# Kernel tuning notes

Measured on AMD Instinct MI355X. Metric: run time of the kernel, lower is better.

The kernel has to match this reference:

```python
import jax, jax.numpy as jnp
import numpy as np

EPS = 1e-5          # denominator epsilon from module
PROJ_EPS = 4e-3     # geoopt float32 projection epsilon
MIN_NORM = 1e-15


def _sabs(x):
    return jnp.abs(x) + MIN_NORM


def _sign(x):
    # geoopt sign: sign(0) == 1
    return jnp.sign(jnp.sign(x) + 0.5)


def _clamp_abs(x, eps):
    return _sign(x) * jnp.maximum(jnp.abs(x), eps)


def _lambda_x(x, k):
    # conformal factor 2 / (1 + k ||x||^2)
    return 2.0 / jnp.maximum(1.0 + k * jnp.sum(x * x, axis=-1, keepdims=True), MIN_NORM)


def _parallel_transport0back(x, v, k):
    # transport v at x back to the origin: v / (1 + k ||x||^2)
    return v / jnp.maximum(1.0 + k * jnp.sum(x * x, axis=-1, keepdims=True), MIN_NORM)


def _artan_k(x, k):
    sk = jnp.sqrt(_sabs(k))
    hyp = jnp.arctanh(jnp.minimum(sk * x, 1.0 - 1e-7)) / sk   # k < 0
    sph = jnp.arctan(sk * x) / sk                              # k > 0
    return jnp.where(k < 0, hyp, sph)


def _tan_k(x, k):
    sk = jnp.sqrt(_sabs(k))
    return jnp.where(k < 0, jnp.tanh(sk * x) / sk, jnp.tan(sk * x) / sk)


def _project(x, k):
    maxnorm = (1.0 - PROJ_EPS) / jnp.sqrt(_sabs(k))
    maxnorm = jnp.where(k < 0, maxnorm, 1e15)
    norm = jnp.maximum(jnp.linalg.norm(x, axis=-1, keepdims=True), MIN_NORM)
    return jnp.where(norm > maxnorm, x / norm * maxnorm, x)


def _mobius_scalar_mul(r, x, k):
    xn = jnp.maximum(jnp.linalg.norm(x, axis=-1, keepdims=True), MIN_NORM)
    return _tan_k(r * _artan_k(xn, k), k) * (x / xn)


def setup_inputs() -> dict:
    key = jax.random.key(0)
    kQ, kK, kV = jax.random.split(key, 3)
    B, H, N, D = 4, 16, 4096, 64
    Q = jax.random.normal(kQ, (B, H, N, D), dtype=jnp.float32)
    K = jax.random.normal(kK, (B, H, N, D), dtype=jnp.float32)
    # V holds points on the Poincare ball: scale so ||V|| < 1
    V = 0.05 * jax.random.normal(kV, (B, H, N, D), dtype=jnp.float32)
    mask = jnp.ones((N,), dtype=jnp.float32)
    c = jnp.array([-1.0], dtype=jnp.float32)  # hyperbolic curvature (geoopt k-convention)
    return {"Q": Q, "K": K, "V": V, "mask": mask, "c": c}


def reference(Q, K, V, mask, c):
    H = Q.shape[-3]
    curv = jnp.broadcast_to(c.reshape(-1), (H,)) if c.shape[0] == 1 else c
    curv = curv[:, None, None]  # [H,1,1] broadcasts over [B,H,N,D]

    x = V
    v1 = _parallel_transport0back(x, Q, curv)
    v2 = _parallel_transport0back(x, K, curv)
    gamma = _lambda_x(x, curv)                     # [B,H,N,1]
    denom = _clamp_abs(gamma - 1.0, 1e-10)
    m = mask[None, :, None]                        # [1,N,1]
    x = gamma / denom * x * m
    v1 = jax.nn.elu(v1) + 1.0
    v2 = denom * (jax.nn.elu(v2) + 1.0) * m

    v2_sum = jnp.sum(v2, axis=-2)                  # [B,H,D]
    D = jnp.einsum('...nd,...d->...n', v1, v2_sum)
    D_inv = 1.0 / jnp.where(D == 0, EPS, D)
    context = jnp.einsum('...nd,...ne->...de', v2, x)   # [B,H,D,D]
    X = jnp.einsum('...de,...nd,...n->...ne', context, v1, D_inv)

    X = _project(X, curv)
    X = _mobius_scalar_mul(0.5, X, curv)
    X = _project(X, curv)
    return X
```

## Files before the change

kernel.cpp:

```cpp
#include <hip/hip_runtime.h>
#include <math.h>

#define EPS_C      1e-05f
#define PROJ_EPS_C 0.004f
#define MIN_NORM_C 1e-15f

#define NTOK   4096
#define DH     64
#define TILE   64
#define CHUNK  512
#define NCHUNK (NTOK / CHUNK)
#define PADROW 68

__device__ __forceinline__ float elup(float z) {
    return z > 0.f ? z + 1.f : __expf(z);
}

__global__ __launch_bounds__(256) void glin_phase1(
    const float* __restrict__ Kk, const float* __restrict__ Vv,
    const float* __restrict__ mask, const float* __restrict__ cc,
    int csize, int H,
    float* __restrict__ pt_out, float* __restrict__ v2sum_out,
    float* __restrict__ ctx_out)
{
    __shared__ __align__(16) float v2s[TILE][PADROW];
    __shared__ __align__(16) float xss[TILE][PADROW];

    const int bh    = blockIdx.x;
    const int chunk = blockIdx.y;
    const int h     = bh % H;
    const float k   = cc[(csize == 1) ? 0 : h];

    const float* Kp = Kk + (size_t)bh * NTOK * DH;
    const float* Vp = Vv + (size_t)bh * NTOK * DH;
    float* ptp      = pt_out + (size_t)bh * NTOK;

    const int tid = threadIdx.x;
    const int ty  = tid >> 4;
    const int tx  = tid & 15;

    float acc[4][4];
#pragma unroll
    for (int i = 0; i < 4; ++i)
#pragma unroll
        for (int j = 0; j < 4; ++j) acc[i][j] = 0.f;
    float v2acc[4] = {0.f, 0.f, 0.f, 0.f};

    const int tbase = chunk * CHUNK;
    for (int tt = 0; tt < CHUNK; tt += TILE) {
#pragma unroll
        for (int p = 0; p < 4; ++p) {
            int f   = tid + p * 256;
            int row = f >> 4;
            int c4  = f & 15;
            int gtok = tbase + tt + row;
            float4 v4 = *(const float4*)(Vp + (size_t)gtok * DH + c4 * 4);
            float4 k4 = *(const float4*)(Kp + (size_t)gtok * DH + c4 * 4);
            float ss = v4.x * v4.x + v4.y * v4.y + v4.z * v4.z + v4.w * v4.w;
            ss += __shfl_xor(ss, 1);
            ss += __shfl_xor(ss, 2);
            ss += __shfl_xor(ss, 4);
            ss += __shfl_xor(ss, 8);
            float dpt   = fmaxf(1.f + k * ss, MIN_NORM_C);
            float pt    = 1.f / dpt;
            float gamma = 2.f * pt;
            float gm1   = gamma - 1.f;
            float sg    = (gm1 < 0.f) ? -1.f : 1.f;
            float denomG = sg * fmaxf(fabsf(gm1), 1e-10f);
            float m     = mask[gtok];
            float xsc   = gamma / denomG * m;
            float a2    = denomG * m;
            if (c4 == 0) ptp[gtok] = pt;
            float4 xs4;
            xs4.x = v4.x * xsc; xs4.y = v4.y * xsc;
            xs4.z = v4.z * xsc; xs4.w = v4.w * xsc;
            float4 w4;
            w4.x = a2 * elup(k4.x * pt);
            w4.y = a2 * elup(k4.y * pt);
            w4.z = a2 * elup(k4.z * pt);
            w4.w = a2 * elup(k4.w * pt);
            *(float4*)&xss[row][c4 * 4] = xs4;
            *(float4*)&v2s[row][c4 * 4] = w4;
        }
        __syncthreads();
#pragma unroll 4
        for (int t = 0; t < TILE; ++t) {
            float4 a = *(const float4*)&v2s[t][ty * 4];
            float4 b = *(const float4*)&xss[t][tx * 4];
            float av[4] = {a.x, a.y, a.z, a.w};
            float bv[4] = {b.x, b.y, b.z, b.w};
#pragma unroll
            for (int i = 0; i < 4; ++i) {
                v2acc[i] += av[i];
#pragma unroll
                for (int j = 0; j < 4; ++j)
                    acc[i][j] = fmaf(av[i], bv[j], acc[i][j]);
            }
        }
        __syncthreads();
    }

    float* ctx = ctx_out + (size_t)bh * DH * DH;
#pragma unroll
    for (int i = 0; i < 4; ++i)
#pragma unroll
        for (int j = 0; j < 4; ++j)
            atomicAdd(&ctx[(ty * 4 + i) * DH + tx * 4 + j], acc[i][j]);
    if (tx == 0) {
#pragma unroll
        for (int i = 0; i < 4; ++i)
            atomicAdd(&v2sum_out[(size_t)bh * DH + ty * 4 + i], v2acc[i]);
    }
}

__global__ __launch_bounds__(256) void glin_phase2(
    const float* __restrict__ Qq, const float* __restrict__ cc,
    int csize, int H,
    const float* __restrict__ pt_in, const float* __restrict__ v2sum_in,
    const float* __restrict__ ctx_in, float* __restrict__ out)
{
    __shared__ __align__(16) float ctxs[DH][PADROW];
    __shared__ __align__(16) float v1t[DH][PADROW];
    __shared__ __align__(16) float v2sum[DH];
    __shared__ float dinv[TILE];
    __shared__ __align__(16) float ptl[CHUNK];

    const int bh    = blockIdx.x;
    const int chunk = blockIdx.y;
    const int h     = bh % H;
    const float k   = cc[(csize == 1) ? 0 : h];
    const float sk  = sqrtf(fabsf(k) + MIN_NORM_C);
    const float maxnorm = (k < 0.f) ? (1.f - PROJ_EPS_C) / sk : 1e15f;

    const int tid = threadIdx.x;
    const int ty  = tid >> 4;
    const int tx  = tid & 15;

    const float* Qp = Qq + (size_t)bh * NTOK * DH;
    float* outp     = out + (size_t)bh * NTOK * DH;

#pragma unroll
    for (int p = 0; p < 4; ++p) {
        int f = tid + p * 256;
        int d = f >> 4, c4 = f & 15;
        float4 v = *(const float4*)(ctx_in + (size_t)bh * DH * DH + d * DH + c4 * 4);
        *(float4*)&ctxs[d][c4 * 4] = v;
    }
    if (tid < 16) {
        float4 v = *(const float4*)(v2sum_in + (size_t)bh * DH + tid * 4);
        *(float4*)&v2sum[tid * 4] = v;
    }
    if (tid < CHUNK / 4) {
        float4 v = *(const float4*)(pt_in + (size_t)bh * NTOK + chunk * CHUNK + tid * 4);
        *(float4*)&ptl[tid * 4] = v;
    }
    __syncthreads();

    const int tbase = chunk * CHUNK;
    for (int tt = 0; tt < CHUNK; tt += TILE) {
#pragma unroll
        for (int p = 0; p < 4; ++p) {
            int f   = tid + p * 256;
            int row = f >> 4;
            int c4  = f & 15;
            int gtok = tbase + tt + row;
            float4 q4 = *(const float4*)(Qp + (size_t)gtok * DH + c4 * 4);
            float ptv = ptl[tt + row];
            float4 v1;
            v1.x = elup(q4.x * ptv);
            v1.y = elup(q4.y * ptv);
            v1.z = elup(q4.z * ptv);
            v1.w = elup(q4.w * ptv);
            float4 vs = *(const float4*)&v2sum[c4 * 4];
            float dp = v1.x * vs.x + v1.y * vs.y + v1.z * vs.z + v1.w * vs.w;
            dp += __shfl_xor(dp, 1);
            dp += __shfl_xor(dp, 2);
            dp += __shfl_xor(dp, 4);
            dp += __shfl_xor(dp, 8);
            if (c4 == 0) {
                float Dv = (dp == 0.f) ? EPS_C : dp;
                dinv[row] = 1.f / Dv;
            }
            v1t[c4 * 4 + 0][row] = v1.x;
            v1t[c4 * 4 + 1][row] = v1.y;
            v1t[c4 * 4 + 2][row] = v1.z;
            v1t[c4 * 4 + 3][row] = v1.w;
        }
        __syncthreads();
        float acc[4][4];
#pragma unroll
        for (int i = 0; i < 4; ++i)
#pragma unroll
            for (int j = 0; j < 4; ++j) acc[i][j] = 0.f;
#pragma unroll 4
        for (int d = 0; d < DH; ++d) {
            float4 a = *(const float4*)&v1t[d][ty * 4];
            float4 b = *(const float4*)&ctxs[d][tx * 4];
            float av[4] = {a.x, a.y, a.z, a.w};
            float bv[4] = {b.x, b.y, b.z, b.w};
#pragma unroll
            for (int i = 0; i < 4; ++i)
#pragma unroll
                for (int j = 0; j < 4; ++j)
                    acc[i][j] = fmaf(av[i], bv[j], acc[i][j]);
        }
#pragma unroll
        for (int i = 0; i < 4; ++i) {
            int row  = ty * 4 + i;
            float dv = dinv[row];
            float x0 = acc[i][0] * dv;
            float x1 = acc[i][1] * dv;
            float x2 = acc[i][2] * dv;
            float x3 = acc[i][3] * dv;
            float n2 = x0 * x0 + x1 * x1 + x2 * x2 + x3 * x3;
            n2 += __shfl_xor(n2, 1);
            n2 += __shfl_xor(n2, 2);
            n2 += __shfl_xor(n2, 4);
            n2 += __shfl_xor(n2, 8);
            float n  = fmaxf(sqrtf(n2), MIN_NORM_C);
            float scale = 1.f;
            float n1 = n;
            if (n > maxnorm) { scale = maxnorm / n; n1 = maxnorm; }
            float xn = fmaxf(n1, MIN_NORM_C);
            float tval;
            if (k < 0.f) {
                float inner = fminf(sk * xn, 1.f - 1e-7f);
                float ar = atanhf(inner) / sk;
                tval = tanhf(sk * (0.5f * ar)) / sk;
            } else {
                float ar = atanf(sk * xn) / sk;
                tval = tanf(sk * (0.5f * ar)) / sk;
            }
            float s2 = tval / xn;
            scale *= s2;
            float nrm2 = fmaxf(n1 * s2, MIN_NORM_C);
            if (nrm2 > maxnorm) scale *= maxnorm / nrm2;
            float4 o;
            o.x = x0 * scale; o.y = x1 * scale;
            o.z = x2 * scale; o.w = x3 * scale;
            int gtok = tbase + tt + row;
            *(float4*)(outp + (size_t)gtok * DH + tx * 4) = o;
        }
        __syncthreads();
    }
}

extern "C" void kernel_launch(void* const* d_in, const int* in_sizes, int n_in,
                              void* d_out, int out_size, void* d_ws, size_t ws_size,
                              hipStream_t stream)
{
    const float* Q    = (const float*)d_in[0];
    const float* K    = (const float*)d_in[1];
    const float* V    = (const float*)d_in[2];
    const float* mask = (const float*)d_in[3];
    const float* c    = (const float*)d_in[4];
    const int csize   = in_sizes[4];
    const int BH      = in_sizes[0] / (NTOK * DH);
    const int H       = 16;
    float* out        = (float*)d_out;

    float* pt    = (float*)d_ws;
    float* v2sum = pt + (size_t)BH * NTOK;
    float* ctx   = v2sum + (size_t)BH * DH;

    hipMemsetAsync(v2sum, 0,
                   ((size_t)BH * DH + (size_t)BH * DH * DH) * sizeof(float),
                   stream);

    dim3 grid(BH, NCHUNK);
    glin_phase1<<<grid, 256, 0, stream>>>(K, V, mask, c, csize, H, pt, v2sum, ctx);
    glin_phase2<<<grid, 256, 0, stream>>>(Q, c, csize, H, pt, v2sum, ctx, out);
}
```

Before: 318.1 us.

## Shrink token chunk, add occupancy hints, store v1 row-major for vectorized GEMM

Lowers CHUNK from 512 to 128 so each (b,h) is split across four times as many blocks, and adds a min-blocks-per-CU hint of 4 to both kernels' launch bounds. In phase 2, v1 is now written to shared memory row-major as a single float4 store instead of four scattered transposed scalar stores. The inner GEMM is reorganised to read float4 slices along d from both operands, which cuts shared-memory store traffic. The trade-off is more atomicAdd traffic on ctx and v2sum from the extra chunks, and a possible register cap from the occupancy hint.

```diff
diff --git a/kernel.cpp b/kernel.cpp
--- a/kernel.cpp
+++ b/kernel.cpp
@@ -8,7 +8,7 @@
 #define NTOK   4096
 #define DH     64
 #define TILE   64
-#define CHUNK  512
+#define CHUNK  128
 #define NCHUNK (NTOK / CHUNK)
 #define PADROW 68
 
@@ -16,7 +16,7 @@
     return z > 0.f ? z + 1.f : __expf(z);
 }
 
-__global__ __launch_bounds__(256) void glin_phase1(
+__global__ __launch_bounds__(256, 4) void glin_phase1(
     const float* __restrict__ Kk, const float* __restrict__ Vv,
     const float* __restrict__ mask, const float* __restrict__ cc,
     int csize, int H,
@@ -113,14 +113,14 @@
     }
 }
 
-__global__ __launch_bounds__(256) void glin_phase2(
+__global__ __launch_bounds__(256, 4) void glin_phase2(
     const float* __restrict__ Qq, const float* __restrict__ cc,
     int csize, int H,
     const float* __restrict__ pt_in, const float* __restrict__ v2sum_in,
     const float* __restrict__ ctx_in, float* __restrict__ out)
 {
     __shared__ __align__(16) float ctxs[DH][PADROW];
-    __shared__ __align__(16) float v1t[DH][PADROW];
+    __shared__ __align__(16) float v1s[TILE][PADROW];
     __shared__ __align__(16) float v2sum[DH];
     __shared__ float dinv[TILE];
     __shared__ __align__(16) float ptl[CHUNK];
@@ -181,10 +181,7 @@
                 float Dv = (dp == 0.f) ? EPS_C : dp;
                 dinv[row] = 1.f / Dv;
             }
-            v1t[c4 * 4 + 0][row] = v1.x;
-            v1t[c4 * 4 + 1][row] = v1.y;
-            v1t[c4 * 4 + 2][row] = v1.z;
-            v1t[c4 * 4 + 3][row] = v1.w;
+            *(float4*)&v1s[row][c4 * 4] = v1;
         }
         __syncthreads();
         float acc[4][4];
@@ -192,17 +189,23 @@
         for (int i = 0; i < 4; ++i)
 #pragma unroll
             for (int j = 0; j < 4; ++j) acc[i][j] = 0.f;
-#pragma unroll 4
-        for (int d = 0; d < DH; ++d) {
-            float4 a = *(const float4*)&v1t[d][ty * 4];
-            float4 b = *(const float4*)&ctxs[d][tx * 4];
-            float av[4] = {a.x, a.y, a.z, a.w};
-            float bv[4] = {b.x, b.y, b.z, b.w};
-#pragma unroll
-            for (int i = 0; i < 4; ++i)
-#pragma unroll
-                for (int j = 0; j < 4; ++j)
-                    acc[i][j] = fmaf(av[i], bv[j], acc[i][j]);
+#pragma unroll
+        for (int db = 0; db < DH / 4; ++db) {
+            float bv[4][4];
+#pragma unroll
+            for (int u = 0; u < 4; ++u)
+                *(float4*)&bv[u][0] = *(const float4*)&ctxs[db * 4 + u][tx * 4];
+#pragma unroll
+            for (int i = 0; i < 4; ++i) {
+                float4 a = *(const float4*)&v1s[ty * 4 + i][db * 4];
+#pragma unroll
+                for (int j = 0; j < 4; ++j) {
+                    acc[i][j] = fmaf(a.x, bv[0][j], acc[i][j]);
+                    acc[i][j] = fmaf(a.y, bv[1][j], acc[i][j]);
+                    acc[i][j] = fmaf(a.z, bv[2][j], acc[i][j]);
+                    acc[i][j] = fmaf(a.w, bv[3][j], acc[i][j]);
+                }
+            }
         }
 #pragma unroll
         for (int i = 0; i < 4; ++i) {
```

Result: slower. 1.251 ms (+293.1%).
